# Optimization experiments

Measured on AMD Instinct MI355X. Metric: run time of the kernel, lower is better.

## Reference

```python
import jax, jax.numpy as jnp
import numpy as np

BN_EPS = 1e-5
INTERP_EPS = 1e-8


def setup_inputs() -> dict:
    key = jax.random.key(0)
    ks = jax.random.split(key, 8)
    B, N, S, D1, D2 = 8, 8192, 2048, 128, 256
    C_in, C_mid, C_out = D1 + D2, 256, 256
    return {
        "xyz1": jax.random.normal(ks[0], (B, 3, N), dtype=jnp.float32),
        "xyz2": jax.random.normal(ks[1], (B, 3, S), dtype=jnp.float32),
        "points1": jax.random.normal(ks[2], (B, D1, N), dtype=jnp.float32),
        "points2": jax.random.normal(ks[3], (B, D2, S), dtype=jnp.float32),
        "W0": jax.random.normal(ks[4], (C_mid, C_in), dtype=jnp.float32) * (1.0 / np.sqrt(C_in)),
        "b0": jnp.zeros((C_mid,), dtype=jnp.float32),
        "gamma0": jnp.ones((C_mid,), dtype=jnp.float32),
        "beta0": jnp.zeros((C_mid,), dtype=jnp.float32),
        "W1": jax.random.normal(ks[5], (C_out, C_mid), dtype=jnp.float32) * (1.0 / np.sqrt(C_mid)),
        "b1": jnp.zeros((C_out,), dtype=jnp.float32),
    }


def reference(xyz1, xyz2, points1, points2, W0, b0, gamma0, beta0, W1, b1):
    B, _, N = xyz1.shape
    S = xyz2.shape[2]
    x1 = jnp.transpose(xyz1, (0, 2, 1))  # (B, N, 3)
    x2 = jnpp = jnp.transpose(xyz2, (0, 2, 1))  # (B, S, 3)
    # squared distances: (B, N, S)
    d = (jnp.sum(x1 ** 2, -1)[:, :, None]
         + jnp.sum(x2 ** 2, -1)[:, None, :]
         - 2.0 * jnp.einsum('bnc,bsc->bns', x1, x2))
    # 3 nearest neighbors (fused top-3 instead of full sort; same math)
    neg_d, idx = jax.lax.top_k(-d, 3)  # (B, N, 3)
    dists = -neg_d
    recip = 1.0 / (dists + INTERP_EPS)
    weight = recip / jnp.sum(recip, axis=2, keepdims=True)  # (B, N, 3)
    p2t = jnp.transpose(points2, (0, 2, 1))  # (B, S, D2)
    D2 = p2t.shape[-1]
    gathered = jnp.take_along_axis(p2t, idx.reshape(B, N * 3, 1), axis=1).reshape(B, N, 3, D2)
    interp = jnp.einsum('bnkc,bnk->bcn', gathered, weight)  # (B, D2, N)
    new_points = jnp.concatenate([interp, points1], axis=1)  # (B, D2+D1, N)
    # conv0 (1x1) + BatchNorm (train mode, batch stats) + ReLU
    h = jnp.einsum('oc,bcn->bon', W0, new_points) + b0[None, :, None]
    mean = jnp.mean(h, axis=(0, 2), keepdims=True)
    var = jnp.mean((h - mean) ** 2, axis=(0, 2), keepdims=True)  # biased, as torch BN
    h = gamma0[None, :, None] * (h - mean) * jax.lax.rsqrt(var + BN_EPS) + beta0[None, :, None]
    h = jax.nn.relu(h)
    # conv1 (1x1) + Identity (module pairs conv1 with nn.Identity) + ReLU
    h = jnp.einsum('oc,bcn->bon', W1, h) + b1[None, :, None]
    return jax.nn.relu(h)
```

## Files before the change

kernel.cpp:

```cpp
#include <hip/hip_runtime.h>
#include <stdint.h>

constexpr int B = 8, N = 8192, S = 2048, D1 = 128, D2 = 256;
constexpr int CIN = 384, CMID = 256, COUT = 256;

typedef __attribute__((ext_vector_type(8))) _Float16 half8;
typedef __attribute__((ext_vector_type(4))) _Float16 half4;
typedef __attribute__((ext_vector_type(4))) float f32x4;

union HU { uint32_t u; _Float16 h[2]; };


__global__ __launch_bounds__(256) void k_top3a(const float* __restrict__ xyz1,
                                               const float* __restrict__ xyz2,
                                               float* __restrict__ dout) {
  __shared__ float4 Pq[512];
  __shared__ float md[4][3][64];
  __shared__ int mi[4][3][64];
  const int tid = threadIdx.x;
  const int wv = tid >> 6, lane = tid & 63;
  const int b = blockIdx.y;
  const int sp = blockIdx.z;
  const int sbase = sp * 512;
  const int n = blockIdx.x * 64 + lane;
  const float* x1 = xyz1 + (size_t)b * 3 * N;
  const float* x2 = xyz2 + (size_t)b * 3 * S;

  for (int j = tid; j < 512; j += 256) {
    const int s = sbase + j;
    float sx = x2[s], sy = x2[s + S], sz = x2[s + 2 * S];
    Pq[j] = float4{sx, sy, sz, sx * sx + sy * sy + sz * sz};
  }
  const float ax = x1[n], ay = x1[n + N], az = x1[n + 2 * N];
  const float nax = -2.f * ax, nay = -2.f * ay, naz = -2.f * az;
  __syncthreads();

  float e0 = 1e30f, e1 = 1e30f, e2 = 1e30f;
  int j0 = 0, j1 = 0, j2 = 0;
  const int q0 = wv * 128, q1 = q0 + 128;
#pragma unroll 8
  for (int j = q0; j < q1; ++j) {
    const float4 v = Pq[j];
    const float d = fmaf(nax, v.x, fmaf(nay, v.y, fmaf(naz, v.z, v.w)));
    const int s = sbase + j;
    const bool c0 = d < e0, c1 = d < e1, c2 = d < e2;
    const int u2 = c1 ? j1 : s;
    const int u1 = c0 ? j0 : s;
    j2 = c2 ? u2 : j2;
    j1 = c1 ? u1 : j1;
    j0 = c0 ? s : j0;
    e2 = __builtin_amdgcn_fmed3f(e1, e2, d);
    e1 = __builtin_amdgcn_fmed3f(e0, e1, d);
    e0 = fminf(e0, d);
  }
  md[wv][0][lane] = e0; mi[wv][0][lane] = j0;
  md[wv][1][lane] = e1; mi[wv][1][lane] = j1;
  md[wv][2][lane] = e2; mi[wv][2][lane] = j2;
  __syncthreads();
  if (tid < 64) {
    float f0 = md[0][0][tid], f1 = md[0][1][tid], f2 = md[0][2][tid];
    int g0 = mi[0][0][tid], g1 = mi[0][1][tid], g2 = mi[0][2][tid];
#pragma unroll
    for (int w = 1; w < 4; ++w)
#pragma unroll
      for (int k = 0; k < 3; ++k) {
        float d = md[w][k][tid];
        int i = mi[w][k][tid];
        if (d < f2) {
          if (d < f1) {
            f2 = f1; g2 = g1;
            if (d < f0) { f1 = f0; g1 = g0; f0 = d; g0 = i; }
            else        { f1 = d;  g1 = i; }
          } else { f2 = d; g2 = i; }
        }
      }
    const int nm = blockIdx.x * 64 + tid;
    float* cd = dout + ((size_t)(b * 256 + 128)) * 8192;
    uint32_t* ci = (uint32_t*)cd + 98304;
    cd[(sp * 3 + 0) * N + nm] = f0; ci[(sp * 3 + 0) * N + nm] = (uint32_t)g0;
    cd[(sp * 3 + 1) * N + nm] = f1; ci[(sp * 3 + 1) * N + nm] = (uint32_t)g1;
    cd[(sp * 3 + 2) * N + nm] = f2; ci[(sp * 3 + 2) * N + nm] = (uint32_t)g2;
  }
}

__global__ __launch_bounds__(256) void k_top3b(const float* __restrict__ xyz1,
                                               const float* __restrict__ dout,
                                               uint32_t* __restrict__ pw3) {
  const int gid = blockIdx.x * 256 + threadIdx.x;
  const int b = gid >> 13, n = gid & 8191;
  const float* cd = dout + ((size_t)(b * 256 + 128)) * 8192;
  const uint32_t* ci = (const uint32_t*)cd + 98304;
  float f0 = 1e30f, f1 = 1e30f, f2 = 1e30f;
  int g0 = 0, g1 = 0, g2 = 0;
#pragma unroll
  for (int t = 0; t < 12; ++t) {
    float d = cd[(size_t)t * N + n];
    int i = (int)ci[(size_t)t * N + n];
    if (d < f2) {
      if (d < f1) {
        f2 = f1; g2 = g1;
        if (d < f0) { f1 = f0; g1 = g0; f0 = d; g0 = i; }
        else        { f1 = d;  g1 = i; }
      } else { f2 = d; g2 = i; }
    }
  }
  const float* x1 = xyz1 + (size_t)b * 3 * N;
  const float ax = x1[n], ay = x1[n + N], az = x1[n + 2 * N];
  const float rn = ax * ax + ay * ay + az * az;
  float q0 = fmaxf(f0 + rn, 0.f);
  float q1 = fmaxf(f1 + rn, 0.f);
  float q2 = fmaxf(f2 + rn, 0.f);
  float r0 = 1.0f / (q0 + 1e-8f), r1 = 1.0f / (q1 + 1e-8f), r2 = 1.0f / (q2 + 1e-8f);
  float inv = 1.0f / (r0 + r1 + r2);
  auto pack = [](int i, float w) -> uint32_t {
    uint32_t q = (uint32_t)(w * 2097152.0f + 0.5f);
    if (q > 0x1FFFFFu) q = 0x1FFFFFu;
    return ((uint32_t)i << 21) | q;
  };
  size_t base = ((size_t)b * N + n) * 3;
  pw3[base]     = pack(g0, r0 * inv);
  pw3[base + 1] = pack(g1, r1 * inv);
  pw3[base + 2] = pack(g2, r2 * inv);
}

__global__ __launch_bounds__(256) void k_G(const float* __restrict__ points2,
                                           const float* __restrict__ W0,
                                           float* __restrict__ dout) {
  __shared__ half8 A_lds[4][256];
  __shared__ half8 B_lds[4][32];
  __shared__ float CT[32][258];
  const int tid = threadIdx.x;
  const int b = blockIdx.x >> 6;
  const int s0 = (blockIdx.x & 63) * 32;
  f32x4 acc[4][2] = {};
  const int wv = tid >> 6, lane = tid & 63;
  const int ln = lane & 15, quad = lane >> 4;
  const int bn = tid & 31, bkc = tid >> 5;
  const int ar = tid >> 3, ac4 = tid & 7;

  for (int kk = 0; kk < 256; kk += 32) {
    __syncthreads();
#pragma unroll
    for (int p = 0; p < 8; ++p) {
      int row = ar + 32 * p;
      const float4 v = *(const float4*)(W0 + (size_t)row * CIN + kk + ac4 * 4);
      half4 hv = {(_Float16)v.x, (_Float16)v.y, (_Float16)v.z, (_Float16)v.w};
      *(half4*)((_Float16*)&A_lds[ac4 >> 1][row] + (ac4 & 1) * 4) = hv;
    }
    {
      half4 hv;
#pragma unroll
      for (int j = 0; j < 4; ++j)
        hv[j] = (_Float16)points2[((size_t)(b * 256 + kk + bkc * 4 + j)) * S + s0 + bn];
      *(half4*)((_Float16*)&B_lds[bkc >> 1][bn] + (bkc & 1) * 4) = hv;
    }
    __syncthreads();
    half8 af[4], bf[2];
#pragma unroll
    for (int i = 0; i < 4; ++i) af[i] = A_lds[quad][wv * 64 + i * 16 + ln];
#pragma unroll
    for (int j = 0; j < 2; ++j) bf[j] = B_lds[quad][j * 16 + ln];
#pragma unroll
    for (int i = 0; i < 4; ++i)
#pragma unroll
      for (int j = 0; j < 2; ++j)
        acc[i][j] = __builtin_amdgcn_mfma_f32_16x16x32_f16(af[i], bf[j], acc[i][j], 0, 0, 0);
  }
  __syncthreads();
#pragma unroll
  for (int i = 0; i < 4; ++i)
#pragma unroll
    for (int reg = 0; reg < 4; ++reg) {
      int row = wv * 64 + i * 16 + quad * 4 + reg;
#pragma unroll
      for (int j = 0; j < 2; ++j) CT[j * 16 + ln][row] = acc[i][j][reg];
    }
  __syncthreads();
  const int sl = tid >> 3, g = tid & 7;
  float* g0 = dout + ((size_t)(b * 256 + 128)) * 8192 + (size_t)(s0 + sl) * 256 + g * 32;
#pragma unroll
  for (int q = 0; q < 8; ++q)
    *(float4*)(g0 + q * 4) = *(const float4*)&CT[sl][g * 32 + q * 4];
}

__global__ __launch_bounds__(256) void k_interp(const uint32_t* __restrict__ pw3,
                                                const float* __restrict__ dout_c,
                                                uint32_t* __restrict__ dout_u) {
  __shared__ int sidx[96];
  __shared__ float sw[96];
  const int tid = threadIdx.x;
  const int b = blockIdx.x >> 8;
  const int n0 = (blockIdx.x & 255) * 32;
  if (tid < 96) {
    uint32_t p = pw3[((size_t)b * N + n0) * 3 + tid];
    sidx[tid] = (int)(p >> 21);
    sw[tid] = (float)(p & 0x1FFFFFu) * (1.0f / 2097152.0f);
  }
  __syncthreads();
  const int colL = tid >> 3, p = tid & 7;
  const float* Gb = dout_c + ((size_t)(b * 256 + 128)) * 8192;
  float a[32];
#pragma unroll
  for (int q = 0; q < 32; ++q) a[q] = 0.f;
#pragma unroll
  for (int k = 0; k < 3; ++k) {
    int j = sidx[colL * 3 + k];
    float w = sw[colL * 3 + k];
    const float* g = Gb + (size_t)j * 256 + p * 32;
#pragma unroll
    for (int q = 0; q < 8; ++q) {
      float4 v = *(const float4*)(g + q * 4);
      a[q * 4 + 0] += w * v.x; a[q * 4 + 1] += w * v.y;
      a[q * 4 + 2] += w * v.z; a[q * 4 + 3] += w * v.w;
    }
  }
#pragma unroll
  for (int q = 0; q < 16; ++q) {
    int cp = p * 16 + q;
    HU u;
    u.h[0] = (_Float16)a[2 * q];
    u.h[1] = (_Float16)a[2 * q + 1];
    dout_u[((size_t)(b * 256 + cp)) * 8192 + n0 + colL] = u.u;
  }
}

__global__ __launch_bounds__(256) void k_wpack(const float* __restrict__ W0,
                                               const float* __restrict__ W1,
                                               _Float16* __restrict__ W1h,
                                               _Float16* __restrict__ W0h) {
  const int bid = blockIdx.x;
  if (bid < 64) {
    const int gid = bid * 256 + threadIdx.x;
    const float4 v = *(const float4*)(W1 + (size_t)gid * 4);
    half4 h = {(_Float16)v.x, (_Float16)v.y, (_Float16)v.z, (_Float16)v.w};
    *(half4*)(W1h + (size_t)gid * 4) = h;
  } else {
    const int gid = (bid - 64) * 256 + threadIdx.x;
    const int row = gid >> 5, c4 = gid & 31;
    const float4 v = *(const float4*)(W0 + (size_t)row * CIN + 256 + c4 * 4);
    half4 h = {(_Float16)v.x, (_Float16)v.y, (_Float16)v.z, (_Float16)v.w};
    *(half4*)(W0h + (size_t)row * 128 + c4 * 4) = h;
  }
}

__global__ __launch_bounds__(256) void k_h(uint32_t* __restrict__ h2,
                                           float* __restrict__ dpart,
                                           const float* __restrict__ points1,
                                           const _Float16* __restrict__ W0h,
                                           const float* __restrict__ b0) {
  __shared__ half8 B_lds[16][32];
  __shared__ float red_s[256], red_q[256], sb0[256];
  const int tid = threadIdx.x;
  const int b = blockIdx.x >> 8;
  const int cb = blockIdx.x & 255;
  const int n0 = cb * 32;
  sb0[tid] = b0[tid];
  const int wv = tid >> 6, lane = tid & 63;
  const int ln = lane & 15, quad = lane >> 4;

  f32x4 acc[4][2];
#pragma unroll
  for (int i = 0; i < 4; ++i) {
    const int rb = wv * 64 + i * 16 + quad * 4;
    const int cp0 = rb >> 1;
#pragma unroll
    for (int j = 0; j < 2; ++j) {
      const int col = n0 + j * 16 + ln;
      const size_t a0 = ((size_t)(b * 256 + cp0)) * 8192 + col;
      HU ua, ub;
      ua.u = h2[a0];
      ub.u = h2[a0 + 8192];
      acc[i][j][0] = (float)ua.h[0];
      acc[i][j][1] = (float)ua.h[1];
      acc[i][j][2] = (float)ub.h[0];
      acc[i][j][3] = (float)ub.h[1];
    }
  }
  {
    const int col = tid & 31;
    const int kc0 = tid >> 5;
#pragma unroll
    for (int it = 0; it < 2; ++it) {
      const int kc = kc0 + 8 * it;
      half8 hv;
#pragma unroll
      for (int j = 0; j < 8; ++j)
        hv[j] = (_Float16)points1[((size_t)(b * D1 + kc * 8 + j)) * N + n0 + col];
      B_lds[kc][col] = hv;
    }
  }
  __syncthreads();
  for (int kk = 0; kk < 128; kk += 32) {
    half8 af[4], bf[2];
#pragma unroll
    for (int i = 0; i < 4; ++i) {
      const int row = wv * 64 + i * 16 + ln;
      af[i] = *(const half8*)(W0h + (size_t)row * 128 + kk + quad * 8);
    }
#pragma unroll
    for (int j = 0; j < 2; ++j)
      bf[j] = B_lds[(kk >> 3) + quad][j * 16 + ln];
#pragma unroll
    for (int i = 0; i < 4; ++i)
#pragma unroll
      for (int j = 0; j < 2; ++j)
        acc[i][j] = __builtin_amdgcn_mfma_f32_16x16x32_f16(af[i], bf[j], acc[i][j], 0, 0, 0);
  }
#pragma unroll
  for (int i = 0; i < 4; ++i) {
    const int rb = wv * 64 + i * 16 + quad * 4;
    const int cp0 = rb >> 1;
    float rs[4] = {0.f, 0.f, 0.f, 0.f}, rq[4] = {0.f, 0.f, 0.f, 0.f};
#pragma unroll
    for (int j = 0; j < 2; ++j) {
      const int col = n0 + j * 16 + ln;
      const size_t a0 = ((size_t)(b * 256 + cp0)) * 8192 + col;
      _Float16 e0 = (_Float16)(acc[i][j][0] + sb0[rb + 0]);
      _Float16 e1 = (_Float16)(acc[i][j][1] + sb0[rb + 1]);
      _Float16 e2 = (_Float16)(acc[i][j][2] + sb0[rb + 2]);
      _Float16 e3 = (_Float16)(acc[i][j][3] + sb0[rb + 3]);
      HU o0, o1;
      o0.h[0] = e0; o0.h[1] = e1; o1.h[0] = e2; o1.h[1] = e3;
      h2[a0] = o0.u;
      h2[a0 + 8192] = o1.u;
      float f0 = (float)e0, f1 = (float)e1, f2 = (float)e2, f3 = (float)e3;
      rs[0] += f0; rq[0] += f0 * f0;
      rs[1] += f1; rq[1] += f1 * f1;
      rs[2] += f2; rq[2] += f2 * f2;
      rs[3] += f3; rq[3] += f3 * f3;
    }
#pragma unroll
    for (int reg = 0; reg < 4; ++reg) {
      float s = rs[reg], q = rq[reg];
#pragma unroll
      for (int m = 1; m < 16; m <<= 1) {
        s += __shfl_xor(s, m);
        q += __shfl_xor(q, m);
      }
      if (ln == 0) { red_s[rb + reg] = s; red_q[rb + reg] = q; }
    }
  }
  __syncthreads();
  float* part = dpart + ((size_t)(b * 256 + 192)) * 8192 + (size_t)cb * 512;
  part[tid] = red_s[tid];
  part[256 + tid] = red_q[tid];
}

__global__ __launch_bounds__(256) void k_bn(const float* __restrict__ dpart,
                                            const float* __restrict__ gamma,
                                            const float* __restrict__ beta,
                                            float* __restrict__ bna,
                                            float* __restrict__ bnb) {
  const int c = blockIdx.x;
  const int tid = threadIdx.x;
  float s = 0.f, q = 0.f;
#pragma unroll
  for (int u = tid; u < 2048; u += 256) {
    int b = u >> 8, cb = u & 255;
    const float* part = dpart + ((size_t)(b * 256 + 192)) * 8192 + (size_t)cb * 512;
    s += part[c];
    q += part[256 + c];
  }
#pragma unroll
  for (int m = 1; m < 64; m <<= 1) {
    s += __shfl_xor(s, m);
    q += __shfl_xor(q, m);
  }
  __shared__ float ls[4], lq[4];
  if ((tid & 63) == 0) { ls[tid >> 6] = s; lq[tid >> 6] = q; }
  __syncthreads();
  if (tid == 0) {
    float st = ls[0] + ls[1] + ls[2] + ls[3];
    float qt = lq[0] + lq[1] + lq[2] + lq[3];
    const float invn = 1.0f / (float)(B * N);
    float mean = st * invn;
    float var = qt * invn - mean * mean;
    float a = gamma[c] * rsqrtf(var + 1e-5f);
    bna[c] = a;
    bnb[c] = beta[c] - mean * a;
  }
}

__global__ __launch_bounds__(256) void k_fused1(const uint32_t* h2,
                                                const _Float16* __restrict__ W1h,
                                                const float* __restrict__ b1,
                                                const float* __restrict__ bna,
                                                const float* __restrict__ bnb,
                                                float* out) {
  __shared__ uint32_t Hh[32 * 33 * 4];
  __shared__ float sa[256], sb[256], sb1[256];
  const int tid = threadIdx.x;
  const int b = blockIdx.x >> 8;
  const int n0 = (blockIdx.x & 255) * 32;
  sa[tid] = bna[tid]; sb[tid] = bnb[tid]; sb1[tid] = b1[tid];
  __syncthreads();
  {
    const int c4 = tid & 7;
    const int rg = tid >> 3;
#pragma unroll
    for (int q = 0; q < 4; ++q) {
      const int cp = rg + 32 * q;
      const uint4 v = *(const uint4*)&h2[((size_t)(b * 256 + cp)) * 8192 + n0 + c4 * 4];
      const int k0 = 2 * cp;
      const float a0 = sa[k0], a1 = sa[k0 + 1], b0v = sb[k0], b1v = sb[k0 + 1];
      const int kc = cp >> 2, sub = cp & 3;
      const uint32_t vv[4] = {v.x, v.y, v.z, v.w};
#pragma unroll
      for (int m = 0; m < 4; ++m) {
        HU u; u.u = vv[m];
        float v0 = a0 * (float)u.h[0] + b0v;
        float v1 = a1 * (float)u.h[1] + b1v;
        HU o;
        o.h[0] = (_Float16)(v0 > 0.f ? v0 : 0.f);
        o.h[1] = (_Float16)(v1 > 0.f ? v1 : 0.f);
        Hh[((kc * 33) + c4 * 4 + m) * 4 + sub] = o.u;
      }
    }
  }
  __syncthreads();
  f32x4 acc[4][2] = {};
  const int wv = tid >> 6, lane = tid & 63;
  const int ln = lane & 15, quad = lane >> 4;
  for (int kk = 0; kk < 256; kk += 32) {
    half8 af[4], bf[2];
#pragma unroll
    for (int i = 0; i < 4; ++i) {
      int row = wv * 64 + i * 16 + ln;
      af[i] = *(const half8*)(W1h + (size_t)row * CMID + kk + quad * 8);
    }
#pragma unroll
    for (int j = 0; j < 2; ++j)
      bf[j] = *(const half8*)&Hh[(((kk >> 3) + quad) * 33 + j * 16 + ln) * 4];
#pragma unroll
    for (int i = 0; i < 4; ++i)
#pragma unroll
      for (int j = 0; j < 2; ++j)
        acc[i][j] = __builtin_amdgcn_mfma_f32_16x16x32_f16(af[i], bf[j], acc[i][j], 0, 0, 0);
  }
#pragma unroll
  for (int i = 0; i < 4; ++i) {
    const int rb = wv * 64 + i * 16 + quad * 4;
#pragma unroll
    for (int reg = 0; reg < 4; ++reg) {
      int row = rb + reg;
      float bias = sb1[row];
      float* orow = out + ((size_t)(b * 256 + row)) * 8192 + n0;
#pragma unroll
      for (int j = 0; j < 2; ++j)
        orow[j * 16 + ln] = fmaxf(acc[i][j][reg] + bias, 0.f);
    }
  }
}

extern "C" void kernel_launch(void* const* d_in, const int* in_sizes, int n_in,
                              void* d_out, int out_size, void* d_ws, size_t ws_size,
                              hipStream_t stream) {
  const float* xyz1 = (const float*)d_in[0];
  const float* xyz2 = (const float*)d_in[1];
  const float* points1 = (const float*)d_in[2];
  const float* points2 = (const float*)d_in[3];
  const float* W0 = (const float*)d_in[4];
  const float* b0 = (const float*)d_in[5];
  const float* gamma0 = (const float*)d_in[6];
  const float* beta0 = (const float*)d_in[7];
  const float* W1 = (const float*)d_in[8];
  const float* b1 = (const float*)d_in[9];
  float* out = (float*)d_out;

  char* ws = (char*)d_ws;
  float* bna = (float*)ws;
  float* bnb = (float*)(ws + 1024);
  uint32_t* pw3 = (uint32_t*)(ws + 2048);
  _Float16* W1h = (_Float16*)(ws + 2048);
  _Float16* W0h = (_Float16*)(ws + 2048 + 131072);

  k_top3a<<<dim3(N / 64, B, 4), 256, 0, stream>>>(xyz1, xyz2, out);
  k_top3b<<<dim3(B * N / 256), 256, 0, stream>>>(xyz1, out, pw3);
  k_G<<<dim3(B * 64), 256, 0, stream>>>(points2, W0, out);
  k_interp<<<dim3(B * N / 32), 256, 0, stream>>>(pw3, out, (uint32_t*)out);
  k_wpack<<<dim3(96), 256, 0, stream>>>(W0, W1, W1h, W0h);
  k_h<<<dim3(B * N / 32), 256, 0, stream>>>((uint32_t*)out, out, points1, W0h, b0);
  k_bn<<<dim3(256), 256, 0, stream>>>(out, gamma0, beta0, bna, bnb);
  k_fused1<<<dim3(B * N / 32), 256, 0, stream>>>((const uint32_t*)out, W1h, b1,
                                                 bna, bnb, out);
}
```

Before: 309.8 us.

## Fuse top-3 merge into interp kernel and pre-pack W0 slice for G GEMM

Removes the separate k_top3b kernel and moves the final 12-candidate merge and weight computation into k_interp, which reads the partial top-3 lists directly. This drops the packed pw3 index/weight buffer and the fixed-point quantisation of the weights. k_wpack now runs first and also converts the points2 part of W0 to fp16 into a scratch region of the output buffer. k_G then reads A fragments straight from global memory and stages all of its B tile in LDS once, with one barrier instead of two per k step. The scratch offsets in the output buffer were moved to make room, which risks overlapping regions that later kernels write.

```diff
diff --git a/kernel.cpp b/kernel.cpp
--- a/kernel.cpp
+++ b/kernel.cpp
@@ -10,6 +10,32 @@
 
 union HU { uint32_t u; _Float16 h[2]; };
 
+
+__global__ __launch_bounds__(256) void k_wpack(const float* __restrict__ W0,
+                                               const float* __restrict__ W1,
+                                               _Float16* __restrict__ W1h,
+                                               _Float16* __restrict__ W0h,
+                                               _Float16* __restrict__ W0G) {
+  const int bid = blockIdx.x;
+  if (bid < 64) {
+    const int gid = bid * 256 + threadIdx.x;
+    const float4 v = *(const float4*)(W1 + (size_t)gid * 4);
+    half4 h = {(_Float16)v.x, (_Float16)v.y, (_Float16)v.z, (_Float16)v.w};
+    *(half4*)(W1h + (size_t)gid * 4) = h;
+  } else if (bid < 96) {
+    const int gid = (bid - 64) * 256 + threadIdx.x;
+    const int row = gid >> 5, c4 = gid & 31;
+    const float4 v = *(const float4*)(W0 + (size_t)row * CIN + 256 + c4 * 4);
+    half4 h = {(_Float16)v.x, (_Float16)v.y, (_Float16)v.z, (_Float16)v.w};
+    *(half4*)(W0h + (size_t)row * 128 + c4 * 4) = h;
+  } else {
+    const int gid = (bid - 96) * 256 + threadIdx.x;
+    const int row = gid >> 6, c4 = gid & 63;
+    const float4 v = *(const float4*)(W0 + (size_t)row * CIN + c4 * 4);
+    half4 h = {(_Float16)v.x, (_Float16)v.y, (_Float16)v.z, (_Float16)v.w};
+    *(half4*)(W0G + (size_t)row * 256 + c4 * 4) = h;
+  }
+}
 
 __global__ __launch_bounds__(256) void k_top3a(const float* __restrict__ xyz1,
                                                const float* __restrict__ xyz2,
@@ -75,7 +101,7 @@
         }
       }
     const int nm = blockIdx.x * 64 + tid;
-    float* cd = dout + ((size_t)(b * 256 + 128)) * 8192;
+    float* cd = dout + ((size_t)(b * 256 + 208)) * 8192;
     uint32_t* ci = (uint32_t*)cd + 98304;
     cd[(sp * 3 + 0) * N + nm] = f0; ci[(sp * 3 + 0) * N + nm] = (uint32_t)g0;
     cd[(sp * 3 + 1) * N + nm] = f1; ci[(sp * 3 + 1) * N + nm] = (uint32_t)g1;
@@ -83,51 +109,10 @@
   }
 }
 
-__global__ __launch_bounds__(256) void k_top3b(const float* __restrict__ xyz1,
-                                               const float* __restrict__ dout,
-                                               uint32_t* __restrict__ pw3) {
-  const int gid = blockIdx.x * 256 + threadIdx.x;
-  const int b = gid >> 13, n = gid & 8191;
-  const float* cd = dout + ((size_t)(b * 256 + 128)) * 8192;
-  const uint32_t* ci = (const uint32_t*)cd + 98304;
-  float f0 = 1e30f, f1 = 1e30f, f2 = 1e30f;
-  int g0 = 0, g1 = 0, g2 = 0;
-#pragma unroll
-  for (int t = 0; t < 12; ++t) {
-    float d = cd[(size_t)t * N + n];
-    int i = (int)ci[(size_t)t * N + n];
-    if (d < f2) {
-      if (d < f1) {
-        f2 = f1; g2 = g1;
-        if (d < f0) { f1 = f0; g1 = g0; f0 = d; g0 = i; }
-        else        { f1 = d;  g1 = i; }
-      } else { f2 = d; g2 = i; }
-    }
-  }
-  const float* x1 = xyz1 + (size_t)b * 3 * N;
-  const float ax = x1[n], ay = x1[n + N], az = x1[n + 2 * N];
-  const float rn = ax * ax + ay * ay + az * az;
-  float q0 = fmaxf(f0 + rn, 0.f);
-  float q1 = fmaxf(f1 + rn, 0.f);
-  float q2 = fmaxf(f2 + rn, 0.f);
-  float r0 = 1.0f / (q0 + 1e-8f), r1 = 1.0f / (q1 + 1e-8f), r2 = 1.0f / (q2 + 1e-8f);
-  float inv = 1.0f / (r0 + r1 + r2);
-  auto pack = [](int i, float w) -> uint32_t {
-    uint32_t q = (uint32_t)(w * 2097152.0f + 0.5f);
-    if (q > 0x1FFFFFu) q = 0x1FFFFFu;
-    return ((uint32_t)i << 21) | q;
-  };
-  size_t base = ((size_t)b * N + n) * 3;
-  pw3[base]     = pack(g0, r0 * inv);
-  pw3[base + 1] = pack(g1, r1 * inv);
-  pw3[base + 2] = pack(g2, r2 * inv);
-}
-
 __global__ __launch_bounds__(256) void k_G(const float* __restrict__ points2,
-                                           const float* __restrict__ W0,
+                                           const _Float16* __restrict__ W0G,
                                            float* __restrict__ dout) {
-  __shared__ half8 A_lds[4][256];
-  __shared__ half8 B_lds[4][32];
+  __shared__ half8 B_lds[32][32];
   __shared__ float CT[32][258];
   const int tid = threadIdx.x;
   const int b = blockIdx.x >> 6;
@@ -135,38 +120,34 @@
   f32x4 acc[4][2] = {};
   const int wv = tid >> 6, lane = tid & 63;
   const int ln = lane & 15, quad = lane >> 4;
-  const int bn = tid & 31, bkc = tid >> 5;
-  const int ar = tid >> 3, ac4 = tid & 7;
-
+  const int bn = tid & 31, kc0 = tid >> 5;
+
+#pragma unroll
+  for (int it = 0; it < 4; ++it) {
+    const int kc = kc0 + 8 * it;
+    half8 hv;
+#pragma unroll
+    for (int j = 0; j < 8; ++j)
+      hv[j] = (_Float16)points2[((size_t)(b * 256 + kc * 8 + j)) * S + s0 + bn];
+    B_lds[kc][bn] = hv;
+  }
+  __syncthreads();
   for (int kk = 0; kk < 256; kk += 32) {
-    __syncthreads();
-#pragma unroll
-    for (int p = 0; p < 8; ++p) {
-      int row = ar + 32 * p;
-      const float4 v = *(const float4*)(W0 + (size_t)row * CIN + kk + ac4 * 4);
-      half4 hv = {(_Float16)v.x, (_Float16)v.y, (_Float16)v.z, (_Float16)v.w};
-      *(half4*)((_Float16*)&A_lds[ac4 >> 1][row] + (ac4 & 1) * 4) = hv;
-    }
-    {
-      half4 hv;
-#pragma unroll
-      for (int j = 0; j < 4; ++j)
-        hv[j] = (_Float16)points2[((size_t)(b * 256 + kk + bkc * 4 + j)) * S + s0 + bn];
-      *(half4*)((_Float16*)&B_lds[bkc >> 1][bn] + (bkc & 1) * 4) = hv;
-    }
-    __syncthreads();
     half8 af[4], bf[2];
 #pragma unroll
-    for (int i = 0; i < 4; ++i) af[i] = A_lds[quad][wv * 64 + i * 16 + ln];
-#pragma unroll
-    for (int j = 0; j < 2; ++j) bf[j] = B_lds[quad][j * 16 + ln];
+    for (int i = 0; i < 4; ++i) {
+      const int row = wv * 64 + i * 16 + ln;
+      af[i] = *(const half8*)(W0G + (size_t)row * 256 + kk + quad * 8);
+    }
+#pragma unroll
+    for (int j = 0; j < 2; ++j)
+      bf[j] = B_lds[(kk >> 3) + quad][j * 16 + ln];
 #pragma unroll
     for (int i = 0; i < 4; ++i)
 #pragma unroll
       for (int j = 0; j < 2; ++j)
         acc[i][j] = __builtin_amdgcn_mfma_f32_16x16x32_f16(af[i], bf[j], acc[i][j], 0, 0, 0);
   }
-  __syncthreads();
 #pragma unroll
   for (int i = 0; i < 4; ++i)
 #pragma unroll
@@ -183,7 +164,7 @@
     *(float4*)(g0 + q * 4) = *(const float4*)&CT[sl][g * 32 + q * 4];
 }
 
-__global__ __launch_bounds__(256) void k_interp(const uint32_t* __restrict__ pw3,
+__global__ __launch_bounds__(256) void k_interp(const float* __restrict__ xyz1,
                                                 const float* __restrict__ dout_c,
                                                 uint32_t* __restrict__ dout_u) {
   __shared__ int sidx[96];
@@ -191,10 +172,35 @@
   const int tid = threadIdx.x;
   const int b = blockIdx.x >> 8;
   const int n0 = (blockIdx.x & 255) * 32;
-  if (tid < 96) {
-    uint32_t p = pw3[((size_t)b * N + n0) * 3 + tid];
-    sidx[tid] = (int)(p >> 21);
-    sw[tid] = (float)(p & 0x1FFFFFu) * (1.0f / 2097152.0f);
+  if (tid < 32) {
+    const int n = n0 + tid;
+    const float* cd = dout_c + ((size_t)(b * 256 + 208)) * 8192;
+    const uint32_t* ci = (const uint32_t*)cd + 98304;
+    float f0 = 1e30f, f1 = 1e30f, f2 = 1e30f;
+    int g0 = 0, g1 = 0, g2 = 0;
+#pragma unroll
+    for (int t = 0; t < 12; ++t) {
+      float d = cd[(size_t)t * N + n];
+      int i = (int)ci[(size_t)t * N + n];
+      if (d < f2) {
+        if (d < f1) {
+          f2 = f1; g2 = g1;
+          if (d < f0) { f1 = f0; g1 = g0; f0 = d; g0 = i; }
+          else        { f1 = d;  g1 = i; }
+        } else { f2 = d; g2 = i; }
+      }
+    }
+    const float* x1 = xyz1 + (size_t)b * 3 * N;
+    const float ax = x1[n], ay = x1[n + N], az = x1[n + 2 * N];
+    const float rn = ax * ax + ay * ay + az * az;
+    float q0 = fmaxf(f0 + rn, 0.f);
+    float q1 = fmaxf(f1 + rn, 0.f);
+    float q2 = fmaxf(f2 + rn, 0.f);
+    float r0 = 1.0f / (q0 + 1e-8f), r1 = 1.0f / (q1 + 1e-8f), r2 = 1.0f / (q2 + 1e-8f);
+    float inv = 1.0f / (r0 + r1 + r2);
+    sidx[tid * 3 + 0] = g0; sw[tid * 3 + 0] = r0 * inv;
+    sidx[tid * 3 + 1] = g1; sw[tid * 3 + 1] = r1 * inv;
+    sidx[tid * 3 + 2] = g2; sw[tid * 3 + 2] = r2 * inv;
   }
   __syncthreads();
   const int colL = tid >> 3, p = tid & 7;
@@ -221,25 +227,6 @@
     u.h[0] = (_Float16)a[2 * q];
     u.h[1] = (_Float16)a[2 * q + 1];
     dout_u[((size_t)(b * 256 + cp)) * 8192 + n0 + colL] = u.u;
-  }
-}
-
-__global__ __launch_bounds__(256) void k_wpack(const float* __restrict__ W0,
-                                               const float* __restrict__ W1,
-                                               _Float16* __restrict__ W1h,
-                                               _Float16* __restrict__ W0h) {
-  const int bid = blockIdx.x;
-  if (bid < 64) {
-    const int gid = bid * 256 + threadIdx.x;
-    const float4 v = *(const float4*)(W1 + (size_t)gid * 4);
-    half4 h = {(_Float16)v.x, (_Float16)v.y, (_Float16)v.z, (_Float16)v.w};
-    *(half4*)(W1h + (size_t)gid * 4) = h;
-  } else {
-    const int gid = (bid - 64) * 256 + threadIdx.x;
-    const int row = gid >> 5, c4 = gid & 31;
-    const float4 v = *(const float4*)(W0 + (size_t)row * CIN + 256 + c4 * 4);
-    half4 h = {(_Float16)v.x, (_Float16)v.y, (_Float16)v.z, (_Float16)v.w};
-    *(half4*)(W0h + (size_t)row * 128 + c4 * 4) = h;
   }
 }
 
@@ -470,15 +457,14 @@
   char* ws = (char*)d_ws;
   float* bna = (float*)ws;
   float* bnb = (float*)(ws + 1024);
-  uint32_t* pw3 = (uint32_t*)(ws + 2048);
   _Float16* W1h = (_Float16*)(ws + 2048);
   _Float16* W0h = (_Float16*)(ws + 2048 + 131072);
-
+  _Float16* W0G = (_Float16*)(out + (size_t)240 * 8192);
+
+  k_wpack<<<dim3(160), 256, 0, stream>>>(W0, W1, W1h, W0h, W0G);
   k_top3a<<<dim3(N / 64, B, 4), 256, 0, stream>>>(xyz1, xyz2, out);
-  k_top3b<<<dim3(B * N / 256), 256, 0, stream>>>(xyz1, out, pw3);
-  k_G<<<dim3(B * 64), 256, 0, stream>>>(points2, W0, out);
-  k_interp<<<dim3(B * N / 32), 256, 0, stream>>>(pw3, out, (uint32_t*)out);
-  k_wpack<<<dim3(96), 256, 0, stream>>>(W0, W1, W1h, W0h);
+  k_G<<<dim3(B * 64), 256, 0, stream>>>(points2, W0G, out);
+  k_interp<<<dim3(B * N / 32), 256, 0, stream>>>(xyz1, out, (uint32_t*)out);
   k_h<<<dim3(B * N / 32), 256, 0, stream>>>((uint32_t*)out, out, points1, W0h, b0);
   k_bn<<<dim3(256), 256, 0, stream>>>(out, gamma0, beta0, bna, bnb);
   k_fused1<<<dim3(B * N / 32), 256, 0, stream>>>((const uint32_t*)out, W1h, b1,
```

Measured after the change: 305.0 us. Within noise of the previous version (-1.6%).
